# Performance work log

Measured on AMD Instinct MI355X. Metric: run time of the kernel, lower is better.

The kernel has to match this reference:

```python
import jax, jax.numpy as jnp
import numpy as np

ALPHA_LEAKY = 0.2
EPS = 1e-10


def setup_inputs() -> dict:
    key = jax.random.key(0)
    ks = jax.random.split(key, 7)
    Nq, Nk, E, D = 100000, 100000, 1600000, 64
    return {
        "query_nodes": jax.random.normal(ks[0], (Nq, D), dtype=jnp.float32),
        "key_value_nodes": jax.random.normal(ks[1], (Nk, D), dtype=jnp.float32),
        "edge_index": jax.random.randint(ks[2], (2, E), 0, Nq, dtype=jnp.int64),
        "proj_w": jax.random.normal(ks[3], (D, D), dtype=jnp.float32) * 0.1,
        "proj_b": jax.random.normal(ks[4], (D,), dtype=jnp.float32) * 0.1,
        "attend_w": jax.random.normal(ks[5], (1, 2 * D), dtype=jnp.float32) * 0.1,
        "attend_b": jax.random.normal(ks[6], (1,), dtype=jnp.float32) * 0.1,
    }


def reference(query_nodes, key_value_nodes, edge_index, proj_w, proj_b, attend_w, attend_b):
    Nq, D = query_nodes.shape
    qi, ki = edge_index[0], edge_index[1]  # [E], [E]
    # per-edge gathered + projected features (torch Linear: x @ W.T + b)
    query_proj = query_nodes[qi] @ proj_w.T + proj_b      # [E, D]
    kv_proj = key_value_nodes[ki] @ proj_w.T + proj_b     # [E, D]
    # attend(concat([qp, kp])) == qp @ Wq.T + kp @ Wk.T + b  (avoids [E,2D] concat)
    wq, wk = attend_w[:, :D], attend_w[:, D:]
    e = query_proj @ wq[0] + kv_proj @ wk[0] + attend_b[0]  # [E]
    e = jax.nn.leaky_relu(e, negative_slope=ALPHA_LEAKY)
    # segment-wise (per query node) numerically-stable softmax
    e_max = jax.ops.segment_max(e, qi, num_segments=Nq)    # [Nq] (-inf for empty)
    e_exp = jnp.exp(e - e_max[qi])                          # [E]
    e_sum = jax.ops.segment_sum(e_exp, qi, num_segments=Nq)  # [Nq]
    attention = e_exp / (e_sum[qi] + EPS)                   # [E]  (dropout = identity in eval)
    # weighted scatter-add aggregation back to query nodes
    weighted_values = kv_proj * attention[:, None]          # [E, D]
    aggregated_context = jax.ops.segment_sum(weighted_values, qi, num_segments=Nq)  # [Nq, D]
    return aggregated_context
```

## Files before the change

### kernel.cpp

```cpp
#include <hip/hip_runtime.h>

#define ALPHA_LEAKY 0.2f
#define EPS_F 1e-10f

#define BSHIFT 7
#define BRANGE 128
#define NBMAX 1024
#define CHUNK_B 16384
#define KBUF_CAP 3072
#define GC_STRIDE 16

using half4_t = __attribute__((ext_vector_type(4))) _Float16;
using f32x4 = __attribute__((ext_vector_type(4))) float;

__device__ __forceinline__ unsigned short f2bf(float x) {
  unsigned int u = __float_as_uint(x);
  return (unsigned short)((u + 0x7fffu + ((u >> 16) & 1u)) >> 16);
}

__global__ __launch_bounds__(1024) void bin_proj_kernel(
    const int* __restrict__ eq, const int* __restrict__ ek,
    int* __restrict__ gcursor, unsigned int* __restrict__ pairs, int E,
    int NB, int binBlocks,
    const float* __restrict__ qnodes, const float* __restrict__ kvnodes,
    const float* __restrict__ W, const float* __restrict__ pb,
    const float* __restrict__ aw, unsigned int* __restrict__ Kp16,
    float* __restrict__ sq, float* __restrict__ sk,
    int Nq, int Nk, int projBlocks) {
  const int t = threadIdx.x;

  if (blockIdx.x < binBlocks) {
    __shared__ int lcnt[NBMAX];
    __shared__ int lbase[NBMAX];
    for (int i = t; i < NBMAX; i += 1024) lcnt[i] = 0;
    __syncthreads();

    const int cbase = blockIdx.x * CHUNK_B;
    int4 qv[4], kv[4];
#pragma unroll
    for (int j = 0; j < 4; ++j) {
      const int e0 = cbase + (((j << 10) + t) << 2);
      if (e0 + 3 < E) {
        qv[j] = *(const int4*)(eq + e0);
        kv[j] = *(const int4*)(ek + e0);
      } else {
        int tq[4] = {-1, -1, -1, -1}, tk[4] = {0, 0, 0, 0};
        for (int r = 0; r < 4; ++r)
          if (e0 + r < E) { tq[r] = eq[e0 + r]; tk[r] = ek[e0 + r]; }
        qv[j] = make_int4(tq[0], tq[1], tq[2], tq[3]);
        kv[j] = make_int4(tk[0], tk[1], tk[2], tk[3]);
      }
      if (qv[j].x >= 0) atomicAdd(&lcnt[qv[j].x >> BSHIFT], 1);
      if (qv[j].y >= 0) atomicAdd(&lcnt[qv[j].y >> BSHIFT], 1);
      if (qv[j].z >= 0) atomicAdd(&lcnt[qv[j].z >> BSHIFT], 1);
      if (qv[j].w >= 0) atomicAdd(&lcnt[qv[j].w >> BSHIFT], 1);
    }
    __syncthreads();
    for (int i = t; i < NB; i += 1024) {
      lbase[i] = lcnt[i] ? atomicAdd(&gcursor[i * GC_STRIDE], lcnt[i]) : 0;
      lcnt[i] = 0;
    }
    __syncthreads();
#pragma unroll
    for (int j = 0; j < 4; ++j) {
      const int qs[4] = {qv[j].x, qv[j].y, qv[j].z, qv[j].w};
      const int ks[4] = {kv[j].x, kv[j].y, kv[j].z, kv[j].w};
#pragma unroll
      for (int r = 0; r < 4; ++r) {
        if (qs[r] >= 0) {
          const int b = qs[r] >> BSHIFT;
          const int idx = lbase[b] + atomicAdd(&lcnt[b], 1);
          if (idx < KBUF_CAP)
            pairs[(size_t)b * KBUF_CAP + idx] =
                ((unsigned int)(qs[r] & (BRANGE - 1)) << 20) |
                (unsigned int)ks[r];
        }
      }
    }
    return;
  }

  __shared__ float pt0[1024];
  __shared__ __align__(16) float us[64];
  __shared__ float cq_s;
  const int lane = t & 63;
  const int projId = blockIdx.x - binBlocks;
  const int waveId = projId * 16 + (t >> 6);
  const int nWaves = projBlocks * 16;

  {
    const int pd = t & 63, og = t >> 6;
    float s0 = 0.f;
#pragma unroll
    for (int oo = 0; oo < 4; ++oo) {
      const int o = og * 4 + oo;
      s0 = fmaf(aw[o], W[o * 64 + pd], s0);
    }
    pt0[t] = s0;
  }
  __syncthreads();
  if (t < 64) {
    float s = 0.f;
#pragma unroll
    for (int g2 = 0; g2 < 16; ++g2) s += pt0[g2 * 64 + t];
    us[t] = s;
    if (t == 0) {
      float c0 = 0.f;
      for (int o = 0; o < 64; ++o) c0 = fmaf(aw[o], pb[o], c0);
      cq_s = c0;
    }
  }
  __syncthreads();

  {
    const int sub = lane & 15, ng = lane >> 4;
    const float4 uv = ((const float4*)us)[sub];
    const float c = cq_s;
    for (int base = waveId * 4; base < Nq; base += nWaves * 4) {
      const int n = base + ng;
      float s = 0.f;
      if (n < Nq) {
        const float4 x = *(const float4*)(qnodes + (size_t)n * 64 + sub * 4);
        s = x.x * uv.x + x.y * uv.y + x.z * uv.z + x.w * uv.w;
      }
#pragma unroll
      for (int off = 1; off <= 8; off <<= 1) s += __shfl_xor(s, off, 64);
      if (sub == 0 && n < Nq) sq[n] = s + c;
    }
  }

  const int c = lane & 15, g = lane >> 4;

  half4_t Bf[4][4];
  float pbv[4];
#pragma unroll
  for (int nt = 0; nt < 4; ++nt) {
    pbv[nt] = pb[nt * 16 + c];
#pragma unroll
    for (int ks = 0; ks < 4; ++ks) {
      const float4 wv =
          *(const float4*)(W + (size_t)(nt * 16 + c) * 64 + ks * 16 + g * 4);
      half4_t h;
      h[0] = (_Float16)wv.x;
      h[1] = (_Float16)wv.y;
      h[2] = (_Float16)wv.z;
      h[3] = (_Float16)wv.w;
      Bf[nt][ks] = h;
    }
  }
  const float a0 = aw[64 + c], a1 = aw[80 + c], a2 = aw[96 + c],
              a3 = aw[112 + c];

  const int ntiles = (Nk + 15) >> 4;
  for (int tile = waveId; tile < ntiles; tile += nWaves) {
    const int n0 = tile << 4;
    const int arow = n0 + c;
    const bool aok = arow < Nk;
    const float* xr = kvnodes + (size_t)arow * 64 + g * 4;

    half4_t Af[4];
#pragma unroll
    for (int ks = 0; ks < 4; ++ks) {
      const float4 xv =
          aok ? *(const float4*)(xr + ks * 16) : make_float4(0.f, 0.f, 0.f, 0.f);
      half4_t h;
      h[0] = (_Float16)xv.x;
      h[1] = (_Float16)xv.y;
      h[2] = (_Float16)xv.z;
      h[3] = (_Float16)xv.w;
      Af[ks] = h;
    }

    f32x4 acc0 = {pbv[0], pbv[0], pbv[0], pbv[0]};
    f32x4 acc1 = {pbv[1], pbv[1], pbv[1], pbv[1]};
    f32x4 acc2 = {pbv[2], pbv[2], pbv[2], pbv[2]};
    f32x4 acc3 = {pbv[3], pbv[3], pbv[3], pbv[3]};
#pragma unroll
    for (int ks = 0; ks < 4; ++ks) {
      acc0 = __builtin_amdgcn_mfma_f32_16x16x16f16(Af[ks], Bf[0][ks], acc0, 0, 0, 0);
      acc1 = __builtin_amdgcn_mfma_f32_16x16x16f16(Af[ks], Bf[1][ks], acc1, 0, 0, 0);
      acc2 = __builtin_amdgcn_mfma_f32_16x16x16f16(Af[ks], Bf[2][ks], acc2, 0, 0, 0);
      acc3 = __builtin_amdgcn_mfma_f32_16x16x16f16(Af[ks], Bf[3][ks], acc3, 0, 0, 0);
    }

#pragma unroll
    for (int r = 0; r < 4; ++r) {
      const int node = n0 + g * 4 + r;
      if (node < Nk) {
        const unsigned int u0 =
            ((unsigned int)f2bf(acc1[r]) << 16) | f2bf(acc0[r]);
        const unsigned int u1 =
            ((unsigned int)f2bf(acc3[r]) << 16) | f2bf(acc2[r]);
        unsigned int* kp = Kp16 + (size_t)node * 32;
        kp[c] = u0;
        kp[16 + c] = u1;
      }
    }

    float ws0 = acc0[0] * a0 + acc1[0] * a1 + acc2[0] * a2 + acc3[0] * a3;
    float ws1 = acc0[1] * a0 + acc1[1] * a1 + acc2[1] * a2 + acc3[1] * a3;
    float ws2 = acc0[2] * a0 + acc1[2] * a1 + acc2[2] * a2 + acc3[2] * a3;
    float ws3 = acc0[3] * a0 + acc1[3] * a1 + acc2[3] * a2 + acc3[3] * a3;
#pragma unroll
    for (int off = 1; off <= 8; off <<= 1) {
      ws0 += __shfl_xor(ws0, off, 64);
      ws1 += __shfl_xor(ws1, off, 64);
      ws2 += __shfl_xor(ws2, off, 64);
      ws3 += __shfl_xor(ws3, off, 64);
    }
    if (c == 0) {
      const int nb4 = n0 + g * 4;
      if (nb4 + 3 < Nk) {
        *(float4*)(sk + nb4) = make_float4(ws0, ws1, ws2, ws3);
      } else {
        if (nb4 + 0 < Nk) sk[nb4 + 0] = ws0;
        if (nb4 + 1 < Nk) sk[nb4 + 1] = ws1;
        if (nb4 + 2 < Nk) sk[nb4 + 2] = ws2;
        if (nb4 + 3 < Nk) sk[nb4 + 3] = ws3;
      }
    }
  }
}

__global__ __launch_bounds__(512, 6) void sort_agg_kernel(
    const unsigned int* __restrict__ pairs, const int* __restrict__ gcursor,
    const float* __restrict__ sq, const float* __restrict__ sk,
    const float* __restrict__ ab, const unsigned int* __restrict__ Kp16,
    float* __restrict__ out, int Nq) {
  __shared__ int lcnt[BRANGE];
  __shared__ int lcur[BRANGE];
  __shared__ int lstart[BRANGE + 1];
  __shared__ int kibuf[KBUF_CAP];
  __shared__ int wso2[2];

  const int t = threadIdx.x;
  const int b = blockIdx.x >> 1;
  const int pass = blockIdx.x & 1;
  const int qlo = b << BSHIFT;
  int n = gcursor[b * GC_STRIDE];
  if (n > KBUF_CAP) n = KBUF_CAP;
  const size_t base = (size_t)b * KBUF_CAP;

  if (t < BRANGE) lcnt[t] = 0;
  __syncthreads();

  unsigned int pv[6];
  int np = 0;
#pragma unroll
  for (int r = 0; r < 6; ++r) {
    const int i = t + (r << 9);
    if (i < n) { pv[r] = pairs[base + i]; ++np; }
  }
#pragma unroll
  for (int r = 0; r < 6; ++r)
    if (r < np) atomicAdd(&lcnt[pv[r] >> 20], 1);
  __syncthreads();

  const int lane = t & 63, wv = t >> 6;
  int v = 0, x = 0;
  if (t < BRANGE) {
    v = lcnt[t];
    x = v;
#pragma unroll
    for (int off = 1; off < 64; off <<= 1) {
      const int y = __shfl_up(x, off, 64);
      if (lane >= off) x += y;
    }
    if (lane == 63) wso2[wv] = x;
  }
  __syncthreads();
  if (t < BRANGE) {
    const int excl = ((wv == 1) ? wso2[0] : 0) + x - v;
    lstart[t] = excl;
    lcur[t] = excl;
    if (t == BRANGE - 1) lstart[BRANGE] = excl + v;
  }
  __syncthreads();

#pragma unroll
  for (int r = 0; r < 6; ++r)
    if (r < np)
      kibuf[atomicAdd(&lcur[pv[r] >> 20], 1)] = (int)(pv[r] & 0xFFFFFu);
  __syncthreads();

  const int ng = lane >> 3, dg = lane & 7;
  const float abv = ab[0];
  {
    const int l = (pass << 6) + (wv << 3) + ng;
    const int node = qlo + l;
    const bool act = node < Nq;
    const int s = act ? lstart[l] : 0;
    const int e = act ? lstart[l + 1] : 0;
    const float sqn = act ? sq[node] + abv : 0.f;

    float acc[8] = {0.f, 0.f, 0.f, 0.f, 0.f, 0.f, 0.f, 0.f};
    float wsum = 0.f;

#define ACC8(W, U)                                             \
  acc[0] = fmaf(W, __uint_as_float(U.x << 16), acc[0]);        \
  acc[1] = fmaf(W, __uint_as_float(U.x & 0xffff0000u), acc[1]);\
  acc[2] = fmaf(W, __uint_as_float(U.y << 16), acc[2]);        \
  acc[3] = fmaf(W, __uint_as_float(U.y & 0xffff0000u), acc[3]);\
  acc[4] = fmaf(W, __uint_as_float(U.z << 16), acc[4]);        \
  acc[5] = fmaf(W, __uint_as_float(U.z & 0xffff0000u), acc[5]);\
  acc[6] = fmaf(W, __uint_as_float(U.w << 16), acc[6]);        \
  acc[7] = fmaf(W, __uint_as_float(U.w & 0xffff0000u), acc[7]);

    int j = s;
    for (; j + 8 <= e; j += 8) {
      const int k0 = kibuf[j + 0], k1 = kibuf[j + 1];
      const int k2 = kibuf[j + 2], k3 = kibuf[j + 3];
      const int k4 = kibuf[j + 4], k5 = kibuf[j + 5];
      const int k6 = kibuf[j + 6], k7 = kibuf[j + 7];
      const float e0 = sk[k0], e1 = sk[k1], e2 = sk[k2], e3 = sk[k3];
      const float e4 = sk[k4], e5 = sk[k5], e6 = sk[k6], e7 = sk[k7];
      const uint4 u0 = *(const uint4*)(Kp16 + (size_t)k0 * 32 + (dg << 2));
      const uint4 u1 = *(const uint4*)(Kp16 + (size_t)k1 * 32 + (dg << 2));
      const uint4 u2 = *(const uint4*)(Kp16 + (size_t)k2 * 32 + (dg << 2));
      const uint4 u3 = *(const uint4*)(Kp16 + (size_t)k3 * 32 + (dg << 2));
      const uint4 u4 = *(const uint4*)(Kp16 + (size_t)k4 * 32 + (dg << 2));
      const uint4 u5 = *(const uint4*)(Kp16 + (size_t)k5 * 32 + (dg << 2));
      const uint4 u6 = *(const uint4*)(Kp16 + (size_t)k6 * 32 + (dg << 2));
      const uint4 u7 = *(const uint4*)(Kp16 + (size_t)k7 * 32 + (dg << 2));

      float x0 = sqn + e0; x0 = x0 > 0.f ? x0 : ALPHA_LEAKY * x0;
      float x1 = sqn + e1; x1 = x1 > 0.f ? x1 : ALPHA_LEAKY * x1;
      float x2 = sqn + e2; x2 = x2 > 0.f ? x2 : ALPHA_LEAKY * x2;
      float x3 = sqn + e3; x3 = x3 > 0.f ? x3 : ALPHA_LEAKY * x3;
      float x4 = sqn + e4; x4 = x4 > 0.f ? x4 : ALPHA_LEAKY * x4;
      float x5 = sqn + e5; x5 = x5 > 0.f ? x5 : ALPHA_LEAKY * x5;
      float x6 = sqn + e6; x6 = x6 > 0.f ? x6 : ALPHA_LEAKY * x6;
      float x7 = sqn + e7; x7 = x7 > 0.f ? x7 : ALPHA_LEAKY * x7;
      const float w0 = __expf(x0), w1 = __expf(x1);
      const float w2 = __expf(x2), w3 = __expf(x3);
      const float w4 = __expf(x4), w5 = __expf(x5);
      const float w6 = __expf(x6), w7 = __expf(x7);

      ACC8(w0, u0) ACC8(w1, u1) ACC8(w2, u2) ACC8(w3, u3)
      ACC8(w4, u4) ACC8(w5, u5) ACC8(w6, u6) ACC8(w7, u7)
      wsum += ((w0 + w1) + (w2 + w3)) + ((w4 + w5) + (w6 + w7));
    }
    const int jm = e - 1;
    for (; j < e; j += 4) {
      const int ka = kibuf[j];
      const int kb = kibuf[min(j + 1, jm)];
      const int kc = kibuf[min(j + 2, jm)];
      const int kd = kibuf[min(j + 3, jm)];
      const float ea = sk[ka], eb = sk[kb], ec = sk[kc], ed = sk[kd];
      const uint4 ua = *(const uint4*)(Kp16 + (size_t)ka * 32 + (dg << 2));
      const uint4 ub = *(const uint4*)(Kp16 + (size_t)kb * 32 + (dg << 2));
      const uint4 uc = *(const uint4*)(Kp16 + (size_t)kc * 32 + (dg << 2));
      const uint4 ud = *(const uint4*)(Kp16 + (size_t)kd * 32 + (dg << 2));

      float xa = sqn + ea; xa = xa > 0.f ? xa : ALPHA_LEAKY * xa;
      float xb = sqn + eb; xb = xb > 0.f ? xb : ALPHA_LEAKY * xb;
      float xc = sqn + ec; xc = xc > 0.f ? xc : ALPHA_LEAKY * xc;
      float xd = sqn + ed; xd = xd > 0.f ? xd : ALPHA_LEAKY * xd;
      const float wa = __expf(xa);
      const float wb = (j + 1 < e) ? __expf(xb) : 0.f;
      const float wc = (j + 2 < e) ? __expf(xc) : 0.f;
      const float wd = (j + 3 < e) ? __expf(xd) : 0.f;

      ACC8(wa, ua) ACC8(wb, ub) ACC8(wc, uc) ACC8(wd, ud)
      wsum += (wa + wb) + (wc + wd);
    }
#undef ACC8

    if (act) {
      const float inv = 1.0f / (wsum + EPS_F);
      const int obase = ((dg & 3) << 2) + ((dg >> 2) << 5);
      float4 r0 = {acc[0] * inv, acc[2] * inv, acc[4] * inv, acc[6] * inv};
      float4 r1 = {acc[1] * inv, acc[3] * inv, acc[5] * inv, acc[7] * inv};
      float* o = out + (size_t)node * 64 + obase;
      *(float4*)o = r0;
      *(float4*)(o + 16) = r1;
    }
  }
}

extern "C" void kernel_launch(void* const* d_in, const int* in_sizes, int n_in,
                              void* d_out, int out_size, void* d_ws, size_t ws_size,
                              hipStream_t stream) {
  const float* qnodes = (const float*)d_in[0];
  const float* kvnodes = (const float*)d_in[1];
  const int* ei = (const int*)d_in[2];
  const float* W = (const float*)d_in[3];
  const float* pb = (const float*)d_in[4];
  const float* aw = (const float*)d_in[5];
  const float* ab = (const float*)d_in[6];

  const int Nq = in_sizes[0] / 64;
  const int Nk = in_sizes[1] / 64;
  const int E = in_sizes[2] / 2;
  const int NB = (Nq + BRANGE - 1) >> BSHIFT;

  const int* eq = ei;
  const int* ek = ei + E;

  char* ws = (char*)d_ws;
  unsigned int* pairs = (unsigned int*)ws;
  unsigned int* Kp16 = pairs + (size_t)NBMAX * KBUF_CAP;
  float* sq = (float*)(Kp16 + (size_t)Nk * 32);
  float* sk = sq + Nq;
  int* gcursor = (int*)(sk + Nk);

  hipMemsetAsync(gcursor, 0, NBMAX * GC_STRIDE * sizeof(int), stream);

  const int binBlocks = (E + CHUNK_B - 1) / CHUNK_B;
  const int projBlocks = 512 - binBlocks;
  bin_proj_kernel<<<binBlocks + projBlocks, 1024, 0, stream>>>(
      eq, ek, gcursor, pairs, E, NB, binBlocks, qnodes, kvnodes, W, pb, aw,
      Kp16, sq, sk, Nq, Nk, projBlocks);

  sort_agg_kernel<<<NB * 2, 512, 0, stream>>>(pairs, gcursor, sq, sk, ab,
                                              Kp16, (float*)d_out, Nq);
}
```

Baseline: 168.3 us.

## Halve bin range and interleave binning blocks among projection blocks

Query bins shrink from 128 to 64 nodes, so each sort_agg block handles a single bin in one pass. The old version used two blocks per bin, each re-sorting the same 3072-entry buffer. Binning blocks now sit at every fifth block index, and each loops over chunks in a grid-stride fashion, instead of occupying the first contiguous block indices. The goal is to avoid the duplicated sort work and to spread binning and projection work evenly across CUs. In exchange the per-bin capacity drops to 1536 and the global atomic cursor count doubles. Any bin with more than 1536 edges would silently drop edges.

```diff
diff --git a/kernel.cpp b/kernel.cpp
--- a/kernel.cpp
+++ b/kernel.cpp
@@ -3,12 +3,13 @@
 #define ALPHA_LEAKY 0.2f
 #define EPS_F 1e-10f
 
-#define BSHIFT 7
-#define BRANGE 128
-#define NBMAX 1024
+#define BSHIFT 6
+#define BRANGE 64
+#define NBMAX 2048
 #define CHUNK_B 16384
-#define KBUF_CAP 3072
+#define KBUF_CAP 1536
 #define GC_STRIDE 16
+#define BIN_MOD 5
 
 using half4_t = __attribute__((ext_vector_type(4))) _Float16;
 using f32x4 = __attribute__((ext_vector_type(4))) float;
@@ -21,61 +22,66 @@
 __global__ __launch_bounds__(1024) void bin_proj_kernel(
     const int* __restrict__ eq, const int* __restrict__ ek,
     int* __restrict__ gcursor, unsigned int* __restrict__ pairs, int E,
-    int NB, int binBlocks,
+    int NB, int nBin, int nProj,
     const float* __restrict__ qnodes, const float* __restrict__ kvnodes,
     const float* __restrict__ W, const float* __restrict__ pb,
     const float* __restrict__ aw, unsigned int* __restrict__ Kp16,
-    float* __restrict__ sq, float* __restrict__ sk,
-    int Nq, int Nk, int projBlocks) {
+    float* __restrict__ sq, float* __restrict__ sk, int Nq, int Nk) {
   const int t = threadIdx.x;
 
-  if (blockIdx.x < binBlocks) {
+  if ((blockIdx.x % BIN_MOD) == 0) {
+    const int bb = blockIdx.x / BIN_MOD;
+    const int nch = (E + CHUNK_B - 1) / CHUNK_B;
     __shared__ int lcnt[NBMAX];
     __shared__ int lbase[NBMAX];
-    for (int i = t; i < NBMAX; i += 1024) lcnt[i] = 0;
-    __syncthreads();
-
-    const int cbase = blockIdx.x * CHUNK_B;
-    int4 qv[4], kv[4];
-#pragma unroll
-    for (int j = 0; j < 4; ++j) {
-      const int e0 = cbase + (((j << 10) + t) << 2);
-      if (e0 + 3 < E) {
-        qv[j] = *(const int4*)(eq + e0);
-        kv[j] = *(const int4*)(ek + e0);
-      } else {
-        int tq[4] = {-1, -1, -1, -1}, tk[4] = {0, 0, 0, 0};
-        for (int r = 0; r < 4; ++r)
-          if (e0 + r < E) { tq[r] = eq[e0 + r]; tk[r] = ek[e0 + r]; }
-        qv[j] = make_int4(tq[0], tq[1], tq[2], tq[3]);
-        kv[j] = make_int4(tk[0], tk[1], tk[2], tk[3]);
-      }
-      if (qv[j].x >= 0) atomicAdd(&lcnt[qv[j].x >> BSHIFT], 1);
-      if (qv[j].y >= 0) atomicAdd(&lcnt[qv[j].y >> BSHIFT], 1);
-      if (qv[j].z >= 0) atomicAdd(&lcnt[qv[j].z >> BSHIFT], 1);
-      if (qv[j].w >= 0) atomicAdd(&lcnt[qv[j].w >> BSHIFT], 1);
-    }
-    __syncthreads();
-    for (int i = t; i < NB; i += 1024) {
-      lbase[i] = lcnt[i] ? atomicAdd(&gcursor[i * GC_STRIDE], lcnt[i]) : 0;
-      lcnt[i] = 0;
-    }
-    __syncthreads();
-#pragma unroll
-    for (int j = 0; j < 4; ++j) {
-      const int qs[4] = {qv[j].x, qv[j].y, qv[j].z, qv[j].w};
-      const int ks[4] = {kv[j].x, kv[j].y, kv[j].z, kv[j].w};
-#pragma unroll
-      for (int r = 0; r < 4; ++r) {
-        if (qs[r] >= 0) {
-          const int b = qs[r] >> BSHIFT;
-          const int idx = lbase[b] + atomicAdd(&lcnt[b], 1);
-          if (idx < KBUF_CAP)
-            pairs[(size_t)b * KBUF_CAP + idx] =
-                ((unsigned int)(qs[r] & (BRANGE - 1)) << 20) |
-                (unsigned int)ks[r];
+
+    for (int ch = bb; ch < nch; ch += nBin) {
+      for (int i = t; i < NBMAX; i += 1024) lcnt[i] = 0;
+      __syncthreads();
+
+      const int cbase = ch * CHUNK_B;
+      int4 qv[4], kv[4];
+#pragma unroll
+      for (int j = 0; j < 4; ++j) {
+        const int e0 = cbase + (((j << 10) + t) << 2);
+        if (e0 + 3 < E) {
+          qv[j] = *(const int4*)(eq + e0);
+          kv[j] = *(const int4*)(ek + e0);
+        } else {
+          int tq[4] = {-1, -1, -1, -1}, tk[4] = {0, 0, 0, 0};
+          for (int r = 0; r < 4; ++r)
+            if (e0 + r < E) { tq[r] = eq[e0 + r]; tk[r] = ek[e0 + r]; }
+          qv[j] = make_int4(tq[0], tq[1], tq[2], tq[3]);
+          kv[j] = make_int4(tk[0], tk[1], tk[2], tk[3]);
         }
-      }
+        if (qv[j].x >= 0) atomicAdd(&lcnt[qv[j].x >> BSHIFT], 1);
+        if (qv[j].y >= 0) atomicAdd(&lcnt[qv[j].y >> BSHIFT], 1);
+        if (qv[j].z >= 0) atomicAdd(&lcnt[qv[j].z >> BSHIFT], 1);
+        if (qv[j].w >= 0) atomicAdd(&lcnt[qv[j].w >> BSHIFT], 1);
+      }
+      __syncthreads();
+      for (int i = t; i < NB; i += 1024) {
+        lbase[i] = lcnt[i] ? atomicAdd(&gcursor[i * GC_STRIDE], lcnt[i]) : 0;
+        lcnt[i] = 0;
+      }
+      __syncthreads();
+#pragma unroll
+      for (int j = 0; j < 4; ++j) {
+        const int qs[4] = {qv[j].x, qv[j].y, qv[j].z, qv[j].w};
+        const int ks[4] = {kv[j].x, kv[j].y, kv[j].z, kv[j].w};
+#pragma unroll
+        for (int r = 0; r < 4; ++r) {
+          if (qs[r] >= 0) {
+            const int b = qs[r] >> BSHIFT;
+            const int idx = lbase[b] + atomicAdd(&lcnt[b], 1);
+            if (idx < KBUF_CAP)
+              pairs[(size_t)b * KBUF_CAP + idx] =
+                  ((unsigned int)(qs[r] & (BRANGE - 1)) << 20) |
+                  (unsigned int)ks[r];
+          }
+        }
+      }
+      __syncthreads();
     }
     return;
   }
@@ -84,9 +90,9 @@
   __shared__ __align__(16) float us[64];
   __shared__ float cq_s;
   const int lane = t & 63;
-  const int projId = blockIdx.x - binBlocks;
+  const int projId = blockIdx.x - blockIdx.x / BIN_MOD - 1;
   const int waveId = projId * 16 + (t >> 6);
-  const int nWaves = projBlocks * 16;
+  const int nWaves = nProj * 16;
 
   {
     const int pd = t & 63, og = t >> 6;
@@ -231,11 +237,9 @@
   __shared__ int lcur[BRANGE];
   __shared__ int lstart[BRANGE + 1];
   __shared__ int kibuf[KBUF_CAP];
-  __shared__ int wso2[2];
 
   const int t = threadIdx.x;
-  const int b = blockIdx.x >> 1;
-  const int pass = blockIdx.x & 1;
+  const int b = blockIdx.x;
   const int qlo = b << BSHIFT;
   int n = gcursor[b * GC_STRIDE];
   if (n > KBUF_CAP) n = KBUF_CAP;
@@ -244,33 +248,28 @@
   if (t < BRANGE) lcnt[t] = 0;
   __syncthreads();
 
-  unsigned int pv[6];
+  unsigned int pv[3];
   int np = 0;
 #pragma unroll
-  for (int r = 0; r < 6; ++r) {
+  for (int r = 0; r < 3; ++r) {
     const int i = t + (r << 9);
     if (i < n) { pv[r] = pairs[base + i]; ++np; }
   }
 #pragma unroll
-  for (int r = 0; r < 6; ++r)
+  for (int r = 0; r < 3; ++r)
     if (r < np) atomicAdd(&lcnt[pv[r] >> 20], 1);
   __syncthreads();
 
   const int lane = t & 63, wv = t >> 6;
-  int v = 0, x = 0;
   if (t < BRANGE) {
-    v = lcnt[t];
-    x = v;
+    const int v = lcnt[t];
+    int x = v;
 #pragma unroll
     for (int off = 1; off < 64; off <<= 1) {
       const int y = __shfl_up(x, off, 64);
       if (lane >= off) x += y;
     }
-    if (lane == 63) wso2[wv] = x;
-  }
-  __syncthreads();
-  if (t < BRANGE) {
-    const int excl = ((wv == 1) ? wso2[0] : 0) + x - v;
+    const int excl = x - v;
     lstart[t] = excl;
     lcur[t] = excl;
     if (t == BRANGE - 1) lstart[BRANGE] = excl + v;
@@ -278,7 +277,7 @@
   __syncthreads();
 
 #pragma unroll
-  for (int r = 0; r < 6; ++r)
+  for (int r = 0; r < 3; ++r)
     if (r < np)
       kibuf[atomicAdd(&lcur[pv[r] >> 20], 1)] = (int)(pv[r] & 0xFFFFFu);
   __syncthreads();
@@ -286,7 +285,7 @@
   const int ng = lane >> 3, dg = lane & 7;
   const float abv = ab[0];
   {
-    const int l = (pass << 6) + (wv << 3) + ng;
+    const int l = (wv << 3) + ng;
     const int node = qlo + l;
     const bool act = node < Nq;
     const int s = act ? lstart[l] : 0;
@@ -406,12 +405,13 @@
 
   hipMemsetAsync(gcursor, 0, NBMAX * GC_STRIDE * sizeof(int), stream);
 
-  const int binBlocks = (E + CHUNK_B - 1) / CHUNK_B;
-  const int projBlocks = 512 - binBlocks;
-  bin_proj_kernel<<<binBlocks + projBlocks, 1024, 0, stream>>>(
-      eq, ek, gcursor, pairs, E, NB, binBlocks, qnodes, kvnodes, W, pb, aw,
-      Kp16, sq, sk, Nq, Nk, projBlocks);
-
-  sort_agg_kernel<<<NB * 2, 512, 0, stream>>>(pairs, gcursor, sq, sk, ab,
-                                              Kp16, (float*)d_out, Nq);
+  const int totalBlocks = 512;
+  const int nBin = (totalBlocks + BIN_MOD - 1) / BIN_MOD;
+  const int nProj = totalBlocks - nBin;
+  bin_proj_kernel<<<totalBlocks, 1024, 0, stream>>>(
+      eq, ek, gcursor, pairs, E, NB, nBin, nProj, qnodes, kvnodes, W, pb, aw,
+      Kp16, sq, sk, Nq, Nk);
+
+  sort_agg_kernel<<<NB, 512, 0, stream>>>(pairs, gcursor, sq, sk, ab, Kp16,
+                                          (float*)d_out, Nq);
 }
```

After: 166.9 us. No clear change (-0.8%).
